# Kernel optimization log

Measured on AMD Instinct MI355X. Metric: run time of the kernel, lower is better.

The kernel has to match this reference:

```python
import jax, jax.numpy as jnp
import numpy as np

NUM_RULES = 256
IN_F = 2048
OUT_F = 2048
RANK = 8
BLOCK = 64
NUM_BLOCKS = min(IN_F, OUT_F) // BLOCK  # 32
SHARED_RANK = int(round(np.sqrt(min(IN_F, OUT_F))))  # 45
N = 16384


def setup_inputs() -> dict:
    key = jax.random.key(0)
    ks = jax.random.split(key, 7)
    x = jax.random.normal(ks[0], (N, IN_F), dtype=jnp.float32)
    rule_ids = jax.random.randint(ks[1], (N,), 0, NUM_RULES, dtype=jnp.int32)
    shared_in = jax.random.normal(ks[2], (IN_F, SHARED_RANK), dtype=jnp.float32) * (1.0 / np.sqrt(IN_F))
    shared_out = jax.random.normal(ks[3], (SHARED_RANK, OUT_F), dtype=jnp.float32) * (1.0 / np.sqrt(SHARED_RANK))
    rule_in = jax.random.normal(ks[4], (NUM_RULES, BLOCK, RANK), dtype=jnp.float32) * (1.0 / np.sqrt(BLOCK))
    rule_out = jax.random.normal(ks[5], (NUM_RULES, RANK, BLOCK), dtype=jnp.float32) * (1.0 / np.sqrt(RANK))
    rule_block_logits = jax.random.normal(ks[6], (NUM_RULES, NUM_BLOCKS), dtype=jnp.float32) * (1.0 / np.sqrt(NUM_BLOCKS))
    return {"x": x, "rule_ids": rule_ids, "shared_in": shared_in, "shared_out": shared_out,
            "rule_in": rule_in, "rule_out": rule_out, "rule_block_logits": rule_block_logits}


def reference(x, rule_ids, shared_in, shared_out, rule_in, rule_out, rule_block_logits):
    # Shared low-rank path: [N, in] @ [in, r] @ [r, out]
    base_out = (x @ shared_in) @ shared_out  # [N, OUT_F]

    total = NUM_BLOCKS * BLOCK
    x_blocks = x[:, :total].reshape(-1, NUM_BLOCKS, BLOCK)  # [N, B, bs]

    # Per-token gather of rule adapter params. This is mathematically
    # identical to the torch sort/pad/bmm/scatter path (zero padding
    # contributes zero), expressed as a dense gather + batched einsum.
    r_in = rule_in[rule_ids]    # [N, bs, RANK]
    r_out = rule_out[rule_ids]  # [N, RANK, bs]
    hidden = jnp.einsum('nbs,nsr->nbr', x_blocks, r_in)     # [N, B, RANK]
    adapter = jnp.einsum('nbr,nrs->nbs', hidden, r_out)     # [N, B, bs]

    # Block selector softmax with temperature 1/sqrt(num_blocks)
    inv_temp = jnp.sqrt(jnp.float32(NUM_BLOCKS))
    sel = jax.nn.softmax(rule_block_logits[rule_ids] * inv_temp, axis=-1)  # [N, B]
    weighted = (adapter * sel[:, :, None]).reshape(-1, total)  # [N, total]

    adapter_full = jnp.zeros_like(base_out).at[:, :total].set(weighted.astype(base_out.dtype))
    return base_out + adapter_full
```

## Files before the change

### kernel.cpp

```cpp
#include <hip/hip_runtime.h>
#include <hip/hip_bf16.h>
#include <math.h>

#define NTOK  16384
#define INF   2048
#define OUTF  2048
#define SR    45
#define RANK  8
#define BLK   64
#define NBLK  32
#define NRULE 256
#define NHIST 32
#define MAXSLOT (NTOK + NRULE * 15)
#define NTILE16 (MAXSLOT / 16)

typedef __attribute__((ext_vector_type(8))) short bf16x8;
typedef __attribute__((ext_vector_type(4))) float f32x4;
typedef __attribute__((ext_vector_type(4))) short s16x4;

#define MFMA __builtin_amdgcn_mfma_f32_16x16x32_bf16
#define SBAR() __builtin_amdgcn_sched_barrier(0)

__device__ inline short f2bs(float f) {
    __hip_bfloat16 h = __float2bfloat16(f);
    return *reinterpret_cast<short*>(&h);
}
__device__ inline bf16x8 cvt8(const float4& a, const float4& b) {
    bf16x8 r;
    r[0] = f2bs(a.x); r[1] = f2bs(a.y); r[2] = f2bs(a.z); r[3] = f2bs(a.w);
    r[4] = f2bs(b.x); r[5] = f2bs(b.y); r[6] = f2bs(b.z); r[7] = f2bs(b.w);
    return r;
}

__global__ void kprep_a(const int* __restrict__ rule_ids,
                        const float* __restrict__ shared_in,
                        const float* __restrict__ shared_out,
                        const float* __restrict__ rule_in,
                        const float* __restrict__ rule_out,
                        unsigned short* __restrict__ ssb,
                        unsigned short* __restrict__ sob,
                        unsigned short* __restrict__ rinf,
                        unsigned short* __restrict__ rof,
                        int* __restrict__ ghist_part,
                        int* __restrict__ perm_p,
                        int* __restrict__ srid_p)
{
    if (blockIdx.x < 128) {
        const int tid = blockIdx.x * 256 + threadIdx.x;
        const int stride = 128 * 256;
        for (int idx = tid; idx < 64 * 3 * 512; idx += stride) {
            int ch = idx / 1536, rem = idx - ch * 1536;
            int nf = rem / 512;
            int l = (rem >> 3) & 63, j = idx & 7;
            int k = ch * 32 + ((l >> 4) << 3) + j;
            int col = nf * 16 + (l & 15);
            ssb[idx] = (col < SR) ? (unsigned short)f2bs(shared_in[(size_t)k * SR + col]) : 0;
        }
        for (int idx = tid; idx < 128 * 2 * 512; idx += stride) {
            int CF = idx >> 10;
            int kc = (idx >> 9) & 1;
            int l = (idx >> 3) & 63, j = idx & 7;
            int k = kc * 32 + ((l >> 4) << 3) + j;
            int col = CF * 16 + (l & 15);
            sob[idx] = (k < SR) ? (unsigned short)f2bs(shared_out[(size_t)k * OUTF + col]) : 0;
        }
        for (int idx = tid; idx < NRULE * 2 * 512; idx += stride) {
            int rid = idx >> 10;
            int half = (idx >> 9) & 1;
            int l = (idx >> 3) & 63, j = idx & 7;
            int r = l & 15;
            int s = half * 32 + ((l >> 4) << 3) + j;
            rinf[idx] = (r < RANK) ? (unsigned short)f2bs(rule_in[(size_t)rid * 512 + s * RANK + r]) : 0;
        }
        for (int idx = tid; idx < NRULE * 4 * 512; idx += stride) {
            int rid = idx >> 11;
            int cf = (idx >> 9) & 3;
            int l = (idx >> 3) & 63, j = idx & 7;
            int k = ((l >> 4) << 3) + j;
            int c = cf * 16 + (l & 15);
            rof[idx] = (k < RANK) ? (unsigned short)f2bs(rule_out[(size_t)rid * 512 + k * BLK + c]) : 0;
        }
    } else {
        __shared__ int lh[NRULE];
        const int tid = threadIdx.x;
        const int hb = blockIdx.x - 128;
        lh[tid] = 0;
        __syncthreads();
        const int base = hb * 512;
        atomicAdd(&lh[rule_ids[base + tid]], 1);
        atomicAdd(&lh[rule_ids[base + 256 + tid]], 1);
        __syncthreads();
        ghist_part[hb * NRULE + tid] = lh[tid];
        for (int j = tid; j < MAXSLOT / 32; j += 256) {
            int idx = hb * (MAXSLOT / 32) + j;
            perm_p[idx] = -1;
            srid_p[idx] = 0;
        }
    }
}

__global__ void kprep_scan(const int* __restrict__ ghist_part,
                           const float* __restrict__ logits,
                           int* __restrict__ gcnt,
                           int* __restrict__ srid_p,
                           float* __restrict__ sel_t,
                           int* __restrict__ ntot)
{
    __shared__ int sc[NRULE];
    const int tid = threadIdx.x;
    int h = 0;
#pragma unroll
    for (int b = 0; b < NHIST; ++b) h += ghist_part[b * NRULE + tid];
    const int pd = (h + 15) & ~15;
    sc[tid] = pd;
    for (int off = 1; off < NRULE; off <<= 1) {
        __syncthreads();
        int v = (tid >= off) ? sc[tid - off] : 0;
        __syncthreads();
        sc[tid] += v;
    }
    __syncthreads();
    const int excl = sc[tid] - pd;
    gcnt[tid] = excl;
    for (int q = h; q < pd; ++q) srid_p[excl + q] = tid;
    if (tid == NRULE - 1) *ntot = sc[tid];
    const float invT = 5.65685424949238f;
    const float* __restrict__ lg = logits + (size_t)tid * NBLK;
    float m = -1e30f;
    for (int b = 0; b < NBLK; ++b) m = fmaxf(m, lg[b] * invT);
    float s = 0.0f;
    for (int b = 0; b < NBLK; ++b) s += expf(lg[b] * invT - m);
    const float inv = 1.0f / s;
    for (int b = 0; b < NBLK; ++b)
        sel_t[(size_t)tid * NBLK + b] = expf(lg[b] * invT - m) * inv;
}

__global__ void kprep_scatter(const int* __restrict__ rule_ids,
                              int* __restrict__ gcnt,
                              int* __restrict__ perm_p,
                              int* __restrict__ srid_p)
{
    const int i = blockIdx.x * 256 + threadIdx.x;
    const int r = rule_ids[i];
    const int p = atomicAdd(&gcnt[r], 1);
    perm_p[p] = i;
    srid_p[p] = r;
}

__global__ __launch_bounds__(256, 2)
void kmain(const float* __restrict__ x,
           const int* __restrict__ perm_p,
           const int* __restrict__ srid_p,
           const unsigned short* __restrict__ ssb,
           const unsigned short* __restrict__ sob,
           const unsigned short* __restrict__ rinf,
           const unsigned short* __restrict__ rof,
           const float* __restrict__ sel_t,
           const int* __restrict__ ntot,
           float* __restrict__ out)
{
    __shared__ __align__(16) unsigned short xbf[16 * 2048];
    __shared__ __align__(16) unsigned short hs_lds[16][264];
    __shared__ __align__(16) unsigned short t_bf[16][72];

#define TRD(W, SL, C) (((float*)xbf)[((W) * 16 + (SL)) * 52 + (C)])

    const int slot0 = blockIdx.x * 16;
    if (slot0 >= *ntot) return;

    const int tid  = threadIdx.x;
    const int lane = tid & 63;
    const int w    = tid >> 6;
    const int row_l = lane & 15, grp = lane >> 4;

    const int rid_u = __builtin_amdgcn_readfirstlane(srid_p[slot0]);

    {
        const int sr = tid >> 4;
        const int su = tid & 15;
        int stok = perm_p[slot0 + sr];  if (stok < 0) stok = 0;
        const float* __restrict__ xrow = x + (size_t)stok * INF;
        const int swz = sr & 7;
        unsigned short* __restrict__ xd = xbf + sr * 2048;
#pragma unroll
        for (int j = 0; j < 16; ++j) {
            const int u8 = j * 16 + su;
            const float4 a = *(const float4*)(xrow + (u8 << 3));
            const float4 b = *(const float4*)(xrow + (u8 << 3) + 4);
            *(bf16x8*)(xd + ((u8 ^ swz) << 3)) = cvt8(a, b);
        }
    }

    const bf16x8 ri0 = *(const bf16x8*)(rinf + ((size_t)rid_u * 2 + 0) * 512 + lane * 8);
    const bf16x8 ri1 = *(const bf16x8*)(rinf + ((size_t)rid_u * 2 + 1) * 512 + lane * 8);

    __syncthreads();

    f32x4 aT0 = {0.f, 0.f, 0.f, 0.f};
    f32x4 aT1 = {0.f, 0.f, 0.f, 0.f};
    f32x4 aT2 = {0.f, 0.f, 0.f, 0.f};

    const int xswz = row_l & 7;
    const unsigned short* __restrict__ xrd = xbf + row_l * 2048;

#pragma unroll
    for (int ci = 0; ci < 8; ++ci) {
        const int c = (w << 3) + ci;
        f32x4 aH = {0.f, 0.f, 0.f, 0.f};
#pragma unroll
        for (int s = 0; s < 2; ++s) {
            const int u8 = (c << 3) + (s << 2) + grp;
            const bf16x8 af = *(const bf16x8*)(xrd + ((u8 ^ xswz) << 3));
            const unsigned short* __restrict__ sp =
                ssb + (size_t)(c * 2 + s) * 1536 + lane * 8;
            aT0 = MFMA(af, *(const bf16x8*)(sp),        aT0, 0, 0, 0);
            aT1 = MFMA(af, *(const bf16x8*)(sp + 512),  aT1, 0, 0, 0);
            aT2 = MFMA(af, *(const bf16x8*)(sp + 1024), aT2, 0, 0, 0);
            aH  = MFMA(af, s ? ri1 : ri0, aH, 0, 0, 0);
        }
        const float sel = sel_t[(size_t)rid_u * NBLK + c];
        if (row_l < RANK) {
#pragma unroll
            for (int q = 0; q < 4; ++q)
                hs_lds[(grp << 2) + q][c * 8 + row_l] =
                    (unsigned short)f2bs(aH[q] * sel);
        }
    }
    __syncthreads();

#pragma unroll
    for (int q = 0; q < 4; ++q) {
        const int sl = (grp << 2) + q;
        TRD(w, sl, row_l)      = aT0[q];
        TRD(w, sl, 16 + row_l) = aT1[q];
        TRD(w, sl, 32 + row_l) = aT2[q];
    }
    __syncthreads();
    {
        const int sl = tid >> 4;
        const int c0 = (tid & 15) << 2;
        s16x4 v = {0, 0, 0, 0};
        if (c0 < 48) {
#pragma unroll
            for (int j = 0; j < 4; ++j) {
                const float sm = TRD(0, sl, c0 + j) + TRD(1, sl, c0 + j)
                               + TRD(2, sl, c0 + j) + TRD(3, sl, c0 + j);
                v[j] = f2bs(sm);
            }
        }
        *(s16x4*)(&t_bf[sl][c0]) = v;
    }
    __syncthreads();

    {
        const int p = w;
        const bf16x8 at0 = *(const bf16x8*)(&t_bf[row_l][grp << 3]);
        const bf16x8 at1 = *(const bf16x8*)(&t_bf[row_l][32 + (grp << 3)]);

        bf16x8 rfv[4];
#pragma unroll
        for (int i = 0; i < 4; ++i)
            rfv[i] = *(const bf16x8*)(rof + ((size_t)rid_u * 4 + i) * 512 + lane * 8);

        const int4 pv = *(const int4*)(perm_p + slot0 + (grp << 2));
        float* const orow0 = out + (size_t)(pv.x < 0 ? 0 : pv.x) * OUTF;
        float* const orow1 = out + (size_t)(pv.y < 0 ? 0 : pv.y) * OUTF;
        float* const orow2 = out + (size_t)(pv.z < 0 ? 0 : pv.z) * OUTF;
        float* const orow3 = out + (size_t)(pv.w < 0 ? 0 : pv.w) * OUTF;

        const int CF0 = p * 32;
        const int bb0 = p * 8;
        const unsigned short* __restrict__ sobw = sob + (size_t)CF0 * 1024 + lane * 8;

        bf16x8 sb[4][2];
        bf16x8 ah[2];
        const bf16x8 zz = {0, 0, 0, 0, 0, 0, 0, 0};

#define LOADQ(SL, QI) do { \
        const unsigned short* _sp = sobw + (size_t)(QI) * 1024; \
        sb[SL][0] = *(const bf16x8*)(_sp); \
        sb[SL][1] = *(const bf16x8*)(_sp + 512); \
    } while (0)
#define LOADA(SL, BI) do { \
        ah[SL] = zz; \
        if (lane < 16) \
            ah[SL] = *(const bf16x8*)(&hs_lds[lane][(bb0 + (BI)) * 8]); \
    } while (0)

        LOADQ(0, 0); LOADQ(1, 1); LOADQ(2, 2);
        LOADA(0, 0);
        SBAR();

#pragma unroll
        for (int qi = 0; qi < 32; ++qi) {
            if (qi < 29) LOADQ((qi + 3) & 3, qi + 3);
            if ((qi & 3) == 0 && qi < 28) LOADA(((qi >> 2) + 1) & 1, (qi >> 2) + 1);
            SBAR();
            f32x4 acc = {0.f, 0.f, 0.f, 0.f};
            acc = MFMA(at0, sb[qi & 3][0], acc, 0, 0, 0);
            acc = MFMA(at1, sb[qi & 3][1], acc, 0, 0, 0);
            acc = MFMA(ah[(qi >> 2) & 1], rfv[qi & 3], acc, 0, 0, 0);
            const int col = ((CF0 + qi) << 4) + row_l;
            if (pv.x >= 0) orow0[col] = acc[0];
            if (pv.y >= 0) orow1[col] = acc[1];
            if (pv.z >= 0) orow2[col] = acc[2];
            if (pv.w >= 0) orow3[col] = acc[3];
            SBAR();
        }
#undef LOADQ
#undef LOADA
    }
}

extern "C" void kernel_launch(void* const* d_in, const int* in_sizes, int n_in,
                              void* d_out, int out_size, void* d_ws, size_t ws_size,
                              hipStream_t stream)
{
    const float* x          = (const float*)d_in[0];
    const int*   rule_ids   = (const int*)  d_in[1];
    const float* shared_in  = (const float*)d_in[2];
    const float* shared_out = (const float*)d_in[3];
    const float* rule_in    = (const float*)d_in[4];
    const float* rule_out   = (const float*)d_in[5];
    const float* logits     = (const float*)d_in[6];
    float* out = (float*)d_out;

    char* p = (char*)d_ws;
    auto carve = [&p](size_t bytes) {
        char* r = p;
        p += (bytes + 255) & ~(size_t)255;
        return r;
    };
    int*            perm_p = (int*)carve(MAXSLOT * 4);
    int*            srid_p = (int*)carve(MAXSLOT * 4);
    unsigned short* ssb    = (unsigned short*)carve(64 * 3 * 512 * 2);
    unsigned short* sob    = (unsigned short*)carve(128 * 2 * 512 * 2);
    unsigned short* rinf   = (unsigned short*)carve((size_t)NRULE * 2 * 512 * 2);
    unsigned short* rof    = (unsigned short*)carve((size_t)NRULE * 4 * 512 * 2);
    float*          sel_t  = (float*)carve((size_t)NRULE * NBLK * 4);
    int*            ghistp = (int*)carve((size_t)NHIST * NRULE * 4);
    int*            gcnt   = (int*)carve(NRULE * 4);
    int*            ntot   = (int*)carve(4);

    kprep_a<<<dim3(160), dim3(256), 0, stream>>>(
        rule_ids, shared_in, shared_out, rule_in, rule_out,
        ssb, sob, rinf, rof, ghistp, perm_p, srid_p);
    kprep_scan<<<dim3(1), dim3(256), 0, stream>>>(
        ghistp, logits, gcnt, srid_p, sel_t, ntot);
    kprep_scatter<<<dim3(64), dim3(256), 0, stream>>>(
        rule_ids, gcnt, perm_p, srid_p);
    kmain<<<dim3(NTILE16), dim3(256), 0, stream>>>(
        x, perm_p, srid_p, ssb, sob, rinf, rof, sel_t, ntot, out);
}
```

Baseline: 100.3 us.

## Stream x rows into LDS via async global_load_lds with double-buffered quarters

```diff
diff --git a/kernel.cpp b/kernel.cpp
--- a/kernel.cpp
+++ b/kernel.cpp
@@ -17,6 +17,9 @@
 typedef __attribute__((ext_vector_type(8))) short bf16x8;
 typedef __attribute__((ext_vector_type(4))) float f32x4;
 typedef __attribute__((ext_vector_type(4))) short s16x4;
+
+typedef const __attribute__((address_space(1))) unsigned int GU32;
+typedef __attribute__((address_space(3))) unsigned int LU32;
 
 #define MFMA __builtin_amdgcn_mfma_f32_16x16x32_bf16
 #define SBAR() __builtin_amdgcn_sched_barrier(0)
@@ -159,11 +162,11 @@
            const int* __restrict__ ntot,
            float* __restrict__ out)
 {
-    __shared__ __align__(16) unsigned short xbf[16 * 2048];
+    __shared__ __align__(16) char xq[2][32768];
     __shared__ __align__(16) unsigned short hs_lds[16][264];
     __shared__ __align__(16) unsigned short t_bf[16][72];
 
-#define TRD(W, SL, C) (((float*)xbf)[((W) * 16 + (SL)) * 52 + (C)])
+#define TRD(W, SL, C) (((float*)xq)[((W) * 16 + (SL)) * 52 + (C)])
 
     const int slot0 = blockIdx.x * 16;
     if (slot0 >= *ntot) return;
@@ -175,65 +178,68 @@
 
     const int rid_u = __builtin_amdgcn_readfirstlane(srid_p[slot0]);
 
-    {
-        const int sr = tid >> 4;
-        const int su = tid & 15;
-        int stok = perm_p[slot0 + sr];  if (stok < 0) stok = 0;
-        const float* __restrict__ xrow = x + (size_t)stok * INF;
-        const int swz = sr & 7;
-        unsigned short* __restrict__ xd = xbf + sr * 2048;
-#pragma unroll
-        for (int j = 0; j < 16; ++j) {
-            const int u8 = j * 16 + su;
-            const float4 a = *(const float4*)(xrow + (u8 << 3));
-            const float4 b = *(const float4*)(xrow + (u8 << 3) + 4);
-            *(bf16x8*)(xd + ((u8 ^ swz) << 3)) = cvt8(a, b);
-        }
-    }
+    int tok = perm_p[slot0 + (tid & 15)];  if (tok < 0) tok = 0;
+    const char* gsrc = (const char*)(x + (size_t)tok * INF) + ((tid >> 4) << 4);
+
+#define STAGEQ(Q) do { \
+        char* lb = (char*)xq + (((Q) & 1) << 15) + (w << 10); \
+        const size_t go = (size_t)(Q) * 2048; \
+        _Pragma("unroll") \
+        for (int v = 0; v < 8; ++v) \
+            __builtin_amdgcn_global_load_lds((GU32*)(gsrc + go + v * 256), \
+                                             (LU32*)(lb + v * 4096), 16, 0, 0); \
+    } while (0)
 
     const bf16x8 ri0 = *(const bf16x8*)(rinf + ((size_t)rid_u * 2 + 0) * 512 + lane * 8);
     const bf16x8 ri1 = *(const bf16x8*)(rinf + ((size_t)rid_u * 2 + 1) * 512 + lane * 8);
-
-    __syncthreads();
 
     f32x4 aT0 = {0.f, 0.f, 0.f, 0.f};
     f32x4 aT1 = {0.f, 0.f, 0.f, 0.f};
     f32x4 aT2 = {0.f, 0.f, 0.f, 0.f};
 
-    const int xswz = row_l & 7;
-    const unsigned short* __restrict__ xrd = xbf + row_l * 2048;
-
-#pragma unroll
-    for (int ci = 0; ci < 8; ++ci) {
-        const int c = (w << 3) + ci;
-        f32x4 aH = {0.f, 0.f, 0.f, 0.f};
-#pragma unroll
-        for (int s = 0; s < 2; ++s) {
-            const int u8 = (c << 3) + (s << 2) + grp;
-            const bf16x8 af = *(const bf16x8*)(xrd + ((u8 ^ xswz) << 3));
-            const unsigned short* __restrict__ sp =
-                ssb + (size_t)(c * 2 + s) * 1536 + lane * 8;
-            aT0 = MFMA(af, *(const bf16x8*)(sp),        aT0, 0, 0, 0);
-            aT1 = MFMA(af, *(const bf16x8*)(sp + 512),  aT1, 0, 0, 0);
-            aT2 = MFMA(af, *(const bf16x8*)(sp + 1024), aT2, 0, 0, 0);
-            aH  = MFMA(af, s ? ri1 : ri0, aH, 0, 0, 0);
-        }
-        const float sel = sel_t[(size_t)rid_u * NBLK + c];
-        if (row_l < RANK) {
-#pragma unroll
-            for (int q = 0; q < 4; ++q)
-                hs_lds[(grp << 2) + q][c * 8 + row_l] =
-                    (unsigned short)f2bs(aH[q] * sel);
-        }
-    }
+    STAGEQ(0);
     __syncthreads();
 
 #pragma unroll
     for (int q = 0; q < 4; ++q) {
-        const int sl = (grp << 2) + q;
-        TRD(w, sl, row_l)      = aT0[q];
-        TRD(w, sl, 16 + row_l) = aT1[q];
-        TRD(w, sl, 32 + row_l) = aT2[q];
+        if (q < 3) STAGEQ(q + 1);
+        const char* xb = (const char*)xq + ((q & 1) << 15);
+#pragma unroll
+        for (int cc = 0; cc < 2; ++cc) {
+            const int c_local = (cc << 2) + w;
+            const int c = (q << 3) + c_local;
+            f32x4 aH = {0.f, 0.f, 0.f, 0.f};
+#pragma unroll
+            for (int s = 0; s < 2; ++s) {
+                const int bidx = c_local * 4096 + (2 * s + (grp >> 1)) * 1024
+                               + (grp & 1) * 512 + row_l * 16;
+                const float4 fa = *(const float4*)(xb + bidx);
+                const float4 fb = *(const float4*)(xb + bidx + 256);
+                const bf16x8 af = cvt8(fa, fb);
+                const unsigned short* __restrict__ sp =
+                    ssb + (size_t)(c * 2 + s) * 1536 + lane * 8;
+                aT0 = MFMA(af, *(const bf16x8*)(sp),        aT0, 0, 0, 0);
+                aT1 = MFMA(af, *(const bf16x8*)(sp + 512),  aT1, 0, 0, 0);
+                aT2 = MFMA(af, *(const bf16x8*)(sp + 1024), aT2, 0, 0, 0);
+                aH  = MFMA(af, s ? ri1 : ri0, aH, 0, 0, 0);
+            }
+            const float sel = sel_t[(size_t)rid_u * NBLK + c];
+            if (row_l < RANK) {
+#pragma unroll
+                for (int q4 = 0; q4 < 4; ++q4)
+                    hs_lds[(grp << 2) + q4][c * 8 + row_l] =
+                        (unsigned short)f2bs(aH[q4] * sel);
+            }
+        }
+        __syncthreads();
+    }
+
+#pragma unroll
+    for (int q4 = 0; q4 < 4; ++q4) {
+        const int sl = (grp << 2) + q4;
+        TRD(w, sl, row_l)      = aT0[q4];
+        TRD(w, sl, 16 + row_l) = aT1[q4];
+        TRD(w, sl, 32 + row_l) = aT2[q4];
     }
     __syncthreads();
     {
```

Measured after the change: 111.2 us. 10.9% more time.

## Split main kernel into K-split projection and output kernels with async LDS staging

Applied to the files above, without the earlier changes.

```diff
diff --git a/kernel.cpp b/kernel.cpp
--- a/kernel.cpp
+++ b/kernel.cpp
@@ -18,12 +18,23 @@
 typedef __attribute__((ext_vector_type(4))) float f32x4;
 typedef __attribute__((ext_vector_type(4))) short s16x4;
 
+typedef const __attribute__((address_space(1))) unsigned int GU32;
+typedef __attribute__((address_space(3))) unsigned int LU32;
+
 #define MFMA __builtin_amdgcn_mfma_f32_16x16x32_bf16
 #define SBAR() __builtin_amdgcn_sched_barrier(0)
+
+#define VMCNT(n) do { asm volatile("s_waitcnt vmcnt(" #n ")" ::: "memory"); \
+                      __builtin_amdgcn_sched_barrier(0); } while (0)
+#define GLOAD(dst, ptr) \
+    asm volatile("global_load_dwordx4 %0, %1, off" : "=v"(dst) : "v"(ptr) : "memory")
 
 __device__ inline short f2bs(float f) {
     __hip_bfloat16 h = __float2bfloat16(f);
     return *reinterpret_cast<short*>(&h);
+}
+__device__ inline float bs2f(unsigned short s) {
+    union { unsigned u; float f; } v; v.u = ((unsigned)s) << 16; return v.f;
 }
 __device__ inline bf16x8 cvt8(const float4& a, const float4& b) {
     bf16x8 r;
@@ -147,87 +158,139 @@
     srid_p[p] = r;
 }
 
-__global__ __launch_bounds__(256, 2)
-void kmain(const float* __restrict__ x,
-           const int* __restrict__ perm_p,
-           const int* __restrict__ srid_p,
-           const unsigned short* __restrict__ ssb,
-           const unsigned short* __restrict__ sob,
-           const unsigned short* __restrict__ rinf,
-           const unsigned short* __restrict__ rof,
-           const float* __restrict__ sel_t,
-           const int* __restrict__ ntot,
-           float* __restrict__ out)
-{
-    __shared__ __align__(16) unsigned short xbf[16 * 2048];
-    __shared__ __align__(16) unsigned short hs_lds[16][264];
-    __shared__ __align__(16) unsigned short t_bf[16][72];
-
-#define TRD(W, SL, C) (((float*)xbf)[((W) * 16 + (SL)) * 52 + (C)])
-
-    const int slot0 = blockIdx.x * 16;
+__global__ __launch_bounds__(128, 4)
+void k1(const float* __restrict__ x,
+        const int* __restrict__ perm_p,
+        const int* __restrict__ srid_p,
+        const unsigned short* __restrict__ ssb,
+        const unsigned short* __restrict__ rinf,
+        const float* __restrict__ sel_t,
+        const int* __restrict__ ntot,
+        unsigned short* __restrict__ t_part,
+        unsigned short* __restrict__ hs)
+{
+    __shared__ __align__(16) char xq[16384];
+    __shared__ __align__(16) unsigned short hs_st[2][16][8][8];
+
+#define TRD(W, SL, C) (((float*)xq)[((W) * 16 + (SL)) * 48 + (C)])
+
+    const int bid  = blockIdx.x;
+    const int tile = bid >> 1, kh = bid & 1;
+    const int slot0 = tile * 16;
     if (slot0 >= *ntot) return;
 
     const int tid  = threadIdx.x;
     const int lane = tid & 63;
     const int w    = tid >> 6;
     const int row_l = lane & 15, grp = lane >> 4;
+    const int cbase = kh * 16 + w * 8;
 
     const int rid_u = __builtin_amdgcn_readfirstlane(srid_p[slot0]);
 
+    const char* gsrc0; const char* gsrc1; const char* gsrc2; const char* gsrc3;
     {
-        const int sr = tid >> 4;
-        const int su = tid & 15;
-        int stok = perm_p[slot0 + sr];  if (stok < 0) stok = 0;
-        const float* __restrict__ xrow = x + (size_t)stok * INF;
-        const int swz = sr & 7;
-        unsigned short* __restrict__ xd = xbf + sr * 2048;
-#pragma unroll
-        for (int j = 0; j < 16; ++j) {
-            const int u8 = j * 16 + su;
-            const float4 a = *(const float4*)(xrow + (u8 << 3));
-            const float4 b = *(const float4*)(xrow + (u8 << 3) + 4);
-            *(bf16x8*)(xd + ((u8 ^ swz) << 3)) = cvt8(a, b);
-        }
+        const int u = lane & 15;
+        const char* t[4];
+#pragma unroll
+        for (int v = 0; v < 4; ++v) {
+            const int row = 4 * v + (lane >> 4);
+            int tok = perm_p[slot0 + row];
+            if (tok < 0) tok = 0;
+            t[v] = (const char*)(x + (size_t)tok * INF) + ((u ^ (row & 7)) << 4);
+        }
+        gsrc0 = t[0]; gsrc1 = t[1]; gsrc2 = t[2]; gsrc3 = t[3];
     }
 
     const bf16x8 ri0 = *(const bf16x8*)(rinf + ((size_t)rid_u * 2 + 0) * 512 + lane * 8);
     const bf16x8 ri1 = *(const bf16x8*)(rinf + ((size_t)rid_u * 2 + 1) * 512 + lane * 8);
-
-    __syncthreads();
+    float sel8[8];
+#pragma unroll
+    for (int ci = 0; ci < 8; ++ci)
+        sel8[ci] = sel_t[(size_t)rid_u * NBLK + cbase + ci];
+
+    const int swz = row_l & 7;
+    int offs[2][2];
+#pragma unroll
+    for (int s = 0; s < 2; ++s)
+#pragma unroll
+        for (int e = 0; e < 2; ++e)
+            offs[s][e] = row_l * 256 + (((s * 8 + grp * 2 + e) ^ swz) << 4);
+    const int off00 = offs[0][0], off01 = offs[0][1];
+    const int off10 = offs[1][0], off11 = offs[1][1];
 
     f32x4 aT0 = {0.f, 0.f, 0.f, 0.f};
     f32x4 aT1 = {0.f, 0.f, 0.f, 0.f};
     f32x4 aT2 = {0.f, 0.f, 0.f, 0.f};
-
-    const int xswz = row_l & 7;
-    const unsigned short* __restrict__ xrd = xbf + row_l * 2048;
+    bf16x8 wreg[2][6];
+
+    char* const xw = xq + (w << 13);
+
+#define STAGE(SL, CI) do { \
+        char* _lb = xw + ((SL) << 12); \
+        const size_t _o = (size_t)(cbase + (CI)) << 8; \
+        __builtin_amdgcn_global_load_lds((GU32*)(gsrc0 + _o), (LU32*)_lb,          16, 0, 0); \
+        __builtin_amdgcn_global_load_lds((GU32*)(gsrc1 + _o), (LU32*)(_lb + 1024), 16, 0, 0); \
+        __builtin_amdgcn_global_load_lds((GU32*)(gsrc2 + _o), (LU32*)(_lb + 2048), 16, 0, 0); \
+        __builtin_amdgcn_global_load_lds((GU32*)(gsrc3 + _o), (LU32*)(_lb + 3072), 16, 0, 0); \
+    } while (0)
+
+#define WLOAD(SL, CI) do { \
+        const unsigned short* _w0 = ssb + (size_t)((cbase + (CI)) * 2) * 1536 + lane * 8; \
+        GLOAD(wreg[SL][0], _w0); \
+        GLOAD(wreg[SL][1], _w0 + 512); \
+        GLOAD(wreg[SL][2], _w0 + 1024); \
+        GLOAD(wreg[SL][3], _w0 + 1536); \
+        GLOAD(wreg[SL][4], _w0 + 2048); \
+        GLOAD(wreg[SL][5], _w0 + 2560); \
+    } while (0)
+
+    VMCNT(0);
+
+    STAGE(0, 0); WLOAD(0, 0);
+    STAGE(1, 1); WLOAD(1, 1);
 
 #pragma unroll
     for (int ci = 0; ci < 8; ++ci) {
-        const int c = (w << 3) + ci;
+        if (ci < 7) { VMCNT(10); } else { VMCNT(0); }
+        const int sl = ci & 1;
+        const char* xb = xw + (sl << 12);
         f32x4 aH = {0.f, 0.f, 0.f, 0.f};
-#pragma unroll
-        for (int s = 0; s < 2; ++s) {
-            const int u8 = (c << 3) + (s << 2) + grp;
-            const bf16x8 af = *(const bf16x8*)(xrd + ((u8 ^ xswz) << 3));
-            const unsigned short* __restrict__ sp =
-                ssb + (size_t)(c * 2 + s) * 1536 + lane * 8;
-            aT0 = MFMA(af, *(const bf16x8*)(sp),        aT0, 0, 0, 0);
-            aT1 = MFMA(af, *(const bf16x8*)(sp + 512),  aT1, 0, 0, 0);
-            aT2 = MFMA(af, *(const bf16x8*)(sp + 1024), aT2, 0, 0, 0);
-            aH  = MFMA(af, s ? ri1 : ri0, aH, 0, 0, 0);
-        }
-        const float sel = sel_t[(size_t)rid_u * NBLK + c];
+        {
+            const float4 fa0 = *(const float4*)(xb + off00);
+            const float4 fa1 = *(const float4*)(xb + off01);
+            const bf16x8 af0 = cvt8(fa0, fa1);
+            aT0 = MFMA(af0, wreg[sl][0], aT0, 0, 0, 0);
+            aT1 = MFMA(af0, wreg[sl][1], aT1, 0, 0, 0);
+            aT2 = MFMA(af0, wreg[sl][2], aT2, 0, 0, 0);
+            aH  = MFMA(af0, ri0, aH, 0, 0, 0);
+            const float4 fb0 = *(const float4*)(xb + off10);
+            const float4 fb1 = *(const float4*)(xb + off11);
+            const bf16x8 af1 = cvt8(fb0, fb1);
+            aT0 = MFMA(af1, wreg[sl][3], aT0, 0, 0, 0);
+            aT1 = MFMA(af1, wreg[sl][4], aT1, 0, 0, 0);
+            aT2 = MFMA(af1, wreg[sl][5], aT2, 0, 0, 0);
+            aH  = MFMA(af1, ri1, aH, 0, 0, 0);
+        }
         if (row_l < RANK) {
 #pragma unroll
             for (int q = 0; q < 4; ++q)
-                hs_lds[(grp << 2) + q][c * 8 + row_l] =
-                    (unsigned short)f2bs(aH[q] * sel);
-        }
-    }
+                hs_st[w][(grp << 2) + q][ci][row_l] =
+                    (unsigned short)f2bs(aH[q] * sel8[ci]);
+        }
+        if (ci < 6) { STAGE(sl, ci + 2); WLOAD(sl, ci + 2); }
+    }
+
+    {
+        const unsigned short* src = &hs_st[w][0][0][0] + lane * 16;
+        const bf16x8 h0 = *(const bf16x8*)(src);
+        const bf16x8 h1 = *(const bf16x8*)(src + 8);
+        unsigned short* dst = hs + ((size_t)(slot0 + (lane >> 2))) * 256
+                            + cbase * 8 + (lane & 3) * 16;
+        *(bf16x8*)(dst)     = h0;
+        *(bf16x8*)(dst + 8) = h1;
+    }
+
     __syncthreads();
-
 #pragma unroll
     for (int q = 0; q < 4; ++q) {
         const int sl = (grp << 2) + q;
@@ -237,44 +300,82 @@
     }
     __syncthreads();
     {
-        const int sl = tid >> 4;
-        const int c0 = (tid & 15) << 2;
-        s16x4 v = {0, 0, 0, 0};
-        if (c0 < 48) {
-#pragma unroll
-            for (int j = 0; j < 4; ++j) {
-                const float sm = TRD(0, sl, c0 + j) + TRD(1, sl, c0 + j)
-                               + TRD(2, sl, c0 + j) + TRD(3, sl, c0 + j);
-                v[j] = f2bs(sm);
-            }
-        }
-        *(s16x4*)(&t_bf[sl][c0]) = v;
+        const int tcol = tid >> 1;
+        const int s8   = (tid & 1) * 8;
+        bf16x8 vv;
+#pragma unroll
+        for (int j = 0; j < 8; ++j) {
+            float v = 0.f;
+            if (tcol < 48)
+                v = TRD(0, s8 + j, tcol) + TRD(1, s8 + j, tcol);
+            vv[j] = f2bs(v);
+        }
+        *(bf16x8*)(t_part + ((size_t)(tile * 2 + kh) * 64 + tcol) * 16 + s8) = vv;
+    }
+}
+
+__global__ __launch_bounds__(128, 4)
+void k2(const unsigned short* __restrict__ t_part,
+        const unsigned short* __restrict__ hs,
+        const int* __restrict__ perm_p,
+        const int* __restrict__ srid_p,
+        const unsigned short* __restrict__ sob,
+        const unsigned short* __restrict__ rof,
+        const int* __restrict__ ntot,
+        float* __restrict__ out)
+{
+    __shared__ __align__(16) unsigned short t_bf[16][72];
+
+    const int bid  = blockIdx.x;
+    const int tile = bid >> 1, chf = bid & 1;
+    const int slot0 = tile * 16;
+    if (slot0 >= *ntot) return;
+
+    const int tid  = threadIdx.x;
+    const int lane = tid & 63;
+    const int w    = tid >> 6;
+    const int p    = chf * 2 + w;
+    const int row_l = lane & 15, grp = lane >> 4;
+
+    const int rid_u = __builtin_amdgcn_readfirstlane(srid_p[slot0]);
+
+    {
+        const int slot = tid & 15, tc8 = tid >> 4;
+        const unsigned short* t0 = t_part + ((size_t)(tile * 2 + 0) * 64) * 16;
+        const unsigned short* t1 = t_part + ((size_t)(tile * 2 + 1) * 64) * 16;
+        bf16x8 vv;
+#pragma unroll
+        for (int j = 0; j < 8; ++j) {
+            const int tcol = tc8 * 8 + j;
+            const float v = bs2f(t0[tcol * 16 + slot]) + bs2f(t1[tcol * 16 + slot]);
+            vv[j] = f2bs(v);
+        }
+        *(bf16x8*)(&t_bf[slot][tc8 * 8]) = vv;
     }
     __syncthreads();
 
-    {
-        const int p = w;
-        const bf16x8 at0 = *(const bf16x8*)(&t_bf[row_l][grp << 3]);
-        const bf16x8 at1 = *(const bf16x8*)(&t_bf[row_l][32 + (grp << 3)]);
-
-        bf16x8 rfv[4];
-#pragma unroll
-        for (int i = 0; i < 4; ++i)
-            rfv[i] = *(const bf16x8*)(rof + ((size_t)rid_u * 4 + i) * 512 + lane * 8);
-
-        const int4 pv = *(const int4*)(perm_p + slot0 + (grp << 2));
-        float* const orow0 = out + (size_t)(pv.x < 0 ? 0 : pv.x) * OUTF;
-        float* const orow1 = out + (size_t)(pv.y < 0 ? 0 : pv.y) * OUTF;
-        float* const orow2 = out + (size_t)(pv.z < 0 ? 0 : pv.z) * OUTF;
-        float* const orow3 = out + (size_t)(pv.w < 0 ? 0 : pv.w) * OUTF;
-
-        const int CF0 = p * 32;
-        const int bb0 = p * 8;
-        const unsigned short* __restrict__ sobw = sob + (size_t)CF0 * 1024 + lane * 8;
-
-        bf16x8 sb[4][2];
-        bf16x8 ah[2];
-        const bf16x8 zz = {0, 0, 0, 0, 0, 0, 0, 0};
+    const bf16x8 at0 = *(const bf16x8*)(&t_bf[row_l][grp << 3]);
+    const bf16x8 at1 = *(const bf16x8*)(&t_bf[row_l][32 + (grp << 3)]);
+
+    bf16x8 rfv[4];
+#pragma unroll
+    for (int i = 0; i < 4; ++i)
+        rfv[i] = *(const bf16x8*)(rof + ((size_t)rid_u * 4 + i) * 512 + lane * 8);
+
+    const int4 pv = *(const int4*)(perm_p + slot0 + (grp << 2));
+    float* const orow0 = out + (size_t)(pv.x < 0 ? 0 : pv.x) * OUTF;
+    float* const orow1 = out + (size_t)(pv.y < 0 ? 0 : pv.y) * OUTF;
+    float* const orow2 = out + (size_t)(pv.z < 0 ? 0 : pv.z) * OUTF;
+    float* const orow3 = out + (size_t)(pv.w < 0 ? 0 : pv.w) * OUTF;
+
+    const int CF0 = p * 32;
+    const int bb0 = p * 8;
+    const unsigned short* __restrict__ sobw = sob + (size_t)CF0 * 1024 + lane * 8;
+    const unsigned short* __restrict__ hsw  = hs + (size_t)(slot0 + (lane & 15)) * 256;
+
+    bf16x8 sb[4][2];
+    bf16x8 ah[2];
+    const bf16x8 zz = {0, 0, 0, 0, 0, 0, 0, 0};
 
 #define LOADQ(SL, QI) do { \
         const unsigned short* _sp = sobw + (size_t)(QI) * 1024; \
@@ -284,32 +385,31 @@
 #define LOADA(SL, BI) do { \
         ah[SL] = zz; \
         if (lane < 16) \
-            ah[SL] = *(const bf16x8*)(&hs_lds[lane][(bb0 + (BI)) * 8]); \
+            ah[SL] = *(const bf16x8*)(hsw + (size_t)(bb0 + (BI)) * 8); \
     } while (0)
 
-        LOADQ(0, 0); LOADQ(1, 1); LOADQ(2, 2);
-        LOADA(0, 0);
+    LOADQ(0, 0); LOADQ(1, 1); LOADQ(2, 2);
+    LOADA(0, 0);
+    SBAR();
+
+#pragma unroll
+    for (int qi = 0; qi < 32; ++qi) {
+        if (qi < 29) LOADQ((qi + 3) & 3, qi + 3);
+        if ((qi & 3) == 0 && qi < 28) LOADA(((qi >> 2) + 1) & 1, (qi >> 2) + 1);
         SBAR();
-
-#pragma unroll
-        for (int qi = 0; qi < 32; ++qi) {
-            if (qi < 29) LOADQ((qi + 3) & 3, qi + 3);
-            if ((qi & 3) == 0 && qi < 28) LOADA(((qi >> 2) + 1) & 1, (qi >> 2) + 1);
-            SBAR();
-            f32x4 acc = {0.f, 0.f, 0.f, 0.f};
-            acc = MFMA(at0, sb[qi & 3][0], acc, 0, 0, 0);
-            acc = MFMA(at1, sb[qi & 3][1], acc, 0, 0, 0);
-            acc = MFMA(ah[(qi >> 2) & 1], rfv[qi & 3], acc, 0, 0, 0);
-            const int col = ((CF0 + qi) << 4) + row_l;
-            if (pv.x >= 0) orow0[col] = acc[0];
-            if (pv.y >= 0) orow1[col] = acc[1];
-            if (pv.z >= 0) orow2[col] = acc[2];
-            if (pv.w >= 0) orow3[col] = acc[3];
-            SBAR();
-        }
+        f32x4 acc = {0.f, 0.f, 0.f, 0.f};
+        acc = MFMA(at0, sb[qi & 3][0], acc, 0, 0, 0);
+        acc = MFMA(at1, sb[qi & 3][1], acc, 0, 0, 0);
+        acc = MFMA(ah[(qi >> 2) & 1], rfv[qi & 3], acc, 0, 0, 0);
+        const int col = ((CF0 + qi) << 4) + row_l;
+        if (pv.x >= 0) orow0[col] = acc[0];
+        if (pv.y >= 0) orow1[col] = acc[1];
+        if (pv.z >= 0) orow2[col] = acc[2];
+        if (pv.w >= 0) orow3[col] = acc[3];
+        SBAR();
+    }
 #undef LOADQ
 #undef LOADA
-    }
 }
 
 extern "C" void kernel_launch(void* const* d_in, const int* in_sizes, int n_in,
@@ -341,6 +441,8 @@
     int*            ghistp = (int*)carve((size_t)NHIST * NRULE * 4);
     int*            gcnt   = (int*)carve(NRULE * 4);
     int*            ntot   = (int*)carve(4);
+    unsigned short* t_part = (unsigned short*)carve((size_t)NTILE16 * 2 * 64 * 16 * 2);
+    unsigned short* hs     = (unsigned short*)carve((size_t)MAXSLOT * 256 * 2);
 
     kprep_a<<<dim3(160), dim3(256), 0, stream>>>(
         rule_ids, shared_in, shared_out, rule_in, rule_out,
@@ -349,6 +451,8 @@
         ghistp, logits, gcnt, srid_p, sel_t, ntot);
     kprep_scatter<<<dim3(64), dim3(256), 0, stream>>>(
         rule_ids, gcnt, perm_p, srid_p);
-    kmain<<<dim3(NTILE16), dim3(256), 0, stream>>>(
-        x, perm_p, srid_p, ssb, sob, rinf, rof, sel_t, ntot, out);
-}
+    k1<<<dim3(NTILE16 * 2), dim3(128), 0, stream>>>(
+        x, perm_p, srid_p, ssb, rinf, sel_t, ntot, t_part, hs);
+    k2<<<dim3(NTILE16 * 2), dim3(128), 0, stream>>>(
+        t_part, hs, perm_p, srid_p, sob, rof, ntot, out);
+}
```

Result: no change. 101.7 us (+1.4%).

## Stream x tiles via async global_load_lds double buffer instead of full-row staging

Applied to the files above, without the earlier changes.

```diff
diff --git a/kernel.cpp b/kernel.cpp
--- a/kernel.cpp
+++ b/kernel.cpp
@@ -17,6 +17,9 @@
 typedef __attribute__((ext_vector_type(8))) short bf16x8;
 typedef __attribute__((ext_vector_type(4))) float f32x4;
 typedef __attribute__((ext_vector_type(4))) short s16x4;
+
+typedef const __attribute__((address_space(1))) unsigned int GU32;
+typedef __attribute__((address_space(3))) unsigned int LU32;
 
 #define MFMA __builtin_amdgcn_mfma_f32_16x16x32_bf16
 #define SBAR() __builtin_amdgcn_sched_barrier(0)
@@ -147,7 +150,7 @@
     srid_p[p] = r;
 }
 
-__global__ __launch_bounds__(256, 2)
+__global__ __launch_bounds__(256, 4)
 void kmain(const float* __restrict__ x,
            const int* __restrict__ perm_p,
            const int* __restrict__ srid_p,
@@ -159,11 +162,13 @@
            const int* __restrict__ ntot,
            float* __restrict__ out)
 {
-    __shared__ __align__(16) unsigned short xbf[16 * 2048];
+    __shared__ __align__(16) float xbuf[2][2][1024];
+    __shared__ __align__(16) float hstmp[2][2][2][16][8];
     __shared__ __align__(16) unsigned short hs_lds[16][264];
     __shared__ __align__(16) unsigned short t_bf[16][72];
-
-#define TRD(W, SL, C) (((float*)xbf)[((W) * 16 + (SL)) * 52 + (C)])
+    __shared__ float sel_lds[NBLK];
+
+#define TRD(W, SL, C) (((float*)xbuf)[((W) * 16 + (SL)) * 52 + (C)])
 
     const int slot0 = blockIdx.x * 16;
     if (slot0 >= *ntot) return;
@@ -171,63 +176,79 @@
     const int tid  = threadIdx.x;
     const int lane = tid & 63;
     const int w    = tid >> 6;
+    const int kh   = w & 1;
+    const int par  = w >> 1;
     const int row_l = lane & 15, grp = lane >> 4;
 
     const int rid_u = __builtin_amdgcn_readfirstlane(srid_p[slot0]);
 
-    {
-        const int sr = tid >> 4;
-        const int su = tid & 15;
-        int stok = perm_p[slot0 + sr];  if (stok < 0) stok = 0;
-        const float* __restrict__ xrow = x + (size_t)stok * INF;
-        const int swz = sr & 7;
-        unsigned short* __restrict__ xd = xbf + sr * 2048;
-#pragma unroll
-        for (int j = 0; j < 16; ++j) {
-            const int u8 = j * 16 + su;
-            const float4 a = *(const float4*)(xrow + (u8 << 3));
-            const float4 b = *(const float4*)(xrow + (u8 << 3) + 4);
-            *(bf16x8*)(xd + ((u8 ^ swz) << 3)) = cvt8(a, b);
-        }
-    }
-
-    const bf16x8 ri0 = *(const bf16x8*)(rinf + ((size_t)rid_u * 2 + 0) * 512 + lane * 8);
-    const bf16x8 ri1 = *(const bf16x8*)(rinf + ((size_t)rid_u * 2 + 1) * 512 + lane * 8);
-
-    __syncthreads();
+    const int srow = tid >> 4, su = tid & 15;
+    int stok = perm_p[slot0 + srow];  if (stok < 0) stok = 0;
+    const char* gs = (const char*)(x + (size_t)stok * INF) + ((su ^ (srow & 7)) << 4);
+
+#define STAGE(R) do { \
+        char* lb = (char*)xbuf + (((R) & 1) << 13) + ((tid >> 6) << 10); \
+        __builtin_amdgcn_global_load_lds((GU32*)(gs + (size_t)(2 * (R)) * 256), \
+                                         (LU32*)lb,          16, 0, 0); \
+        __builtin_amdgcn_global_load_lds((GU32*)(gs + (size_t)(2 * (R) + 1) * 256), \
+                                         (LU32*)(lb + 4096), 16, 0, 0); \
+    } while (0)
+
+    const int swz = row_l & 7;
+    const int offA = row_l * 256 + (((kh * 8 + grp * 2 + 0) ^ swz) << 4);
+    const int offB = row_l * 256 + (((kh * 8 + grp * 2 + 1) ^ swz) << 4);
+
+    const bf16x8 ri = *(const bf16x8*)(rinf + ((size_t)rid_u * 2 + kh) * 512 + lane * 8);
+    if (tid < NBLK) sel_lds[tid] = sel_t[(size_t)rid_u * NBLK + tid];
 
     f32x4 aT0 = {0.f, 0.f, 0.f, 0.f};
     f32x4 aT1 = {0.f, 0.f, 0.f, 0.f};
     f32x4 aT2 = {0.f, 0.f, 0.f, 0.f};
 
-    const int xswz = row_l & 7;
-    const unsigned short* __restrict__ xrd = xbf + row_l * 2048;
-
-#pragma unroll
-    for (int ci = 0; ci < 8; ++ci) {
-        const int c = (w << 3) + ci;
-        f32x4 aH = {0.f, 0.f, 0.f, 0.f};
-#pragma unroll
-        for (int s = 0; s < 2; ++s) {
-            const int u8 = (c << 3) + (s << 2) + grp;
-            const bf16x8 af = *(const bf16x8*)(xrd + ((u8 ^ xswz) << 3));
-            const unsigned short* __restrict__ sp =
-                ssb + (size_t)(c * 2 + s) * 1536 + lane * 8;
+    STAGE(0);
+    __syncthreads();
+
+    for (int r = 0; r < 16; ++r) {
+        if (r < 15) STAGE(r + 1);
+        if (r > 0) {
+            const int pb = (r - 1) & 1;
+            const int mc = tid >> 7;
+            const int idx = tid & 127;
+            const int sl = idx >> 3, rr = idx & 7;
+            const int b = 2 * (r - 1) + mc;
+            const float v = hstmp[pb][mc][0][sl][rr] + hstmp[pb][mc][1][sl][rr];
+            hs_lds[sl][b * 8 + rr] = (unsigned short)f2bs(v * sel_lds[b]);
+        }
+        {
+            const int c = 2 * r + par;
+            const char* xb = (const char*)xbuf + ((r & 1) << 13) + (par << 12);
+            const float4 fa = *(const float4*)(xb + offA);
+            const float4 fb = *(const float4*)(xb + offB);
+            const bf16x8 af = cvt8(fa, fb);
+            const unsigned short* sp = ssb + (size_t)(c * 2 + kh) * 1536 + lane * 8;
+            f32x4 aH = {0.f, 0.f, 0.f, 0.f};
             aT0 = MFMA(af, *(const bf16x8*)(sp),        aT0, 0, 0, 0);
             aT1 = MFMA(af, *(const bf16x8*)(sp + 512),  aT1, 0, 0, 0);
             aT2 = MFMA(af, *(const bf16x8*)(sp + 1024), aT2, 0, 0, 0);
-            aH  = MFMA(af, s ? ri1 : ri0, aH, 0, 0, 0);
-        }
-        const float sel = sel_t[(size_t)rid_u * NBLK + c];
-        if (row_l < RANK) {
-#pragma unroll
-            for (int q = 0; q < 4; ++q)
-                hs_lds[(grp << 2) + q][c * 8 + row_l] =
-                    (unsigned short)f2bs(aH[q] * sel);
-        }
-    }
-    __syncthreads();
-
+            aH  = MFMA(af, ri, aH, 0, 0, 0);
+            if (row_l < RANK) {
+#pragma unroll
+                for (int q = 0; q < 4; ++q)
+                    hstmp[r & 1][par][kh][(grp << 2) + q][row_l] = aH[q];
+            }
+        }
+        __syncthreads();
+    }
+
+    {
+        const int pb = 1;
+        const int mc = tid >> 7;
+        const int idx = tid & 127;
+        const int sl = idx >> 3, rr = idx & 7;
+        const int b = 30 + mc;
+        const float v = hstmp[pb][mc][0][sl][rr] + hstmp[pb][mc][1][sl][rr];
+        hs_lds[sl][b * 8 + rr] = (unsigned short)f2bs(v * sel_lds[b]);
+    }
 #pragma unroll
     for (int q = 0; q < 4; ++q) {
         const int sl = (grp << 2) + q;
```

Measured after the change: 89.71 us. 10.6% less time.
